# Kernel optimization log

Measured on AMD Instinct MI355X. Metric: run time of the kernel, lower is better.

The kernel has to match this reference:

```python
import jax, jax.numpy as jnp
import numpy as np

H = 16
D_MODEL = 1024
D_K = D_MODEL // H  # 64
NEG = -1e9


def setup_inputs() -> dict:
    key = jax.random.key(0)
    ks = jax.random.split(key, 9)
    nb, nw = 4, 2048
    Q = jax.random.normal(ks[0], (nb, nw, D_MODEL), dtype=jnp.float32)
    K = jax.random.normal(ks[1], (nb, nw, D_MODEL), dtype=jnp.float32)
    V = jax.random.normal(ks[2], (nb, nw, D_MODEL), dtype=jnp.float32)
    mask = jax.random.randint(ks[3], (nb, nw, nw), 0, 2, dtype=jnp.int32)
    s = 1.0 / np.sqrt(D_MODEL)
    Wq = jax.random.normal(ks[4], (D_MODEL, D_MODEL), dtype=jnp.float32) * s
    Wk = jax.random.normal(ks[5], (D_MODEL, D_MODEL), dtype=jnp.float32) * s
    Wv = jax.random.normal(ks[6], (D_MODEL, D_MODEL), dtype=jnp.float32) * s
    Wo = jax.random.normal(ks[7], (D_MODEL, D_MODEL), dtype=jnp.float32) * s
    return {"Q": Q, "K": K, "V": V, "mask": mask,
            "Wq": Wq, "Wk": Wk, "Wv": Wv, "Wo": Wo}


def reference(Q, K, V, mask, Wq, Wk, Wv, Wo):
    nb, nw, _ = Q.shape
    scaling = jnp.asarray(np.sqrt(D_K), dtype=Q.dtype)
    # nn.Linear(bias=False): y = x @ W.T; split heads -> [nb, h, nw, d_k]
    q = (Q @ Wq.T).reshape(nb, nw, H, D_K).transpose(0, 2, 1, 3)
    k = (K @ Wk.T).reshape(nb, nw, H, D_K).transpose(0, 2, 1, 3)
    v = (V @ Wv.T).reshape(nb, nw, H, D_K).transpose(0, 2, 1, 3)
    scores = jnp.einsum('bhqd,bhkd->bhqk', q, k) / scaling
    # mask broadcast over heads (unsqueeze(1) in torch)
    scores = jnp.where(mask[:, None, :, :] == 0, jnp.asarray(NEG, scores.dtype), scores)
    probs = jax.nn.softmax(scores, axis=-1)
    # dropout is identity in eval mode
    attn = jnp.einsum('bhqk,bhkd->bhqd', probs, v)
    x = attn.transpose(0, 2, 1, 3).reshape(nb, nw, D_MODEL)
    return x @ Wo.T
```

## Files before the change

### kernel.cpp

```cpp
#include <hip/hip_runtime.h>
#include <hip/hip_bf16.h>
#include <cstdint>
#include <cmath>

#define NB 4
#define NW 2048
#define DM 1024
#define NH 16
#define DK 64

typedef __attribute__((ext_vector_type(8))) short bf16x8;
typedef __attribute__((ext_vector_type(4))) float f32x4;
union cvt8 { uint4 u; __hip_bfloat16 h[8]; };

__device__ __forceinline__ void async_ld16(const void* g, void* l) {
  __builtin_amdgcn_global_load_lds((__attribute__((address_space(1))) void*)g,
                                   (__attribute__((address_space(3))) void*)l,
                                   16, 0, 0);
}

__device__ __forceinline__ unsigned short bf16bits(float x) {
  __hip_bfloat16 h = __float2bfloat16(x);
  return *(unsigned short*)&h;
}

__global__ void __launch_bounds__(256) cvt_qkv(const float* __restrict__ Q,
                                               const float* __restrict__ K,
                                               const float* __restrict__ V,
                                               __hip_bfloat16* __restrict__ Qb,
                                               __hip_bfloat16* __restrict__ Kb,
                                               __hip_bfloat16* __restrict__ Vb) {
  const float* in = blockIdx.y == 0 ? Q : (blockIdx.y == 1 ? K : V);
  __hip_bfloat16* out = blockIdx.y == 0 ? Qb : (blockIdx.y == 1 ? Kb : Vb);
  size_t i = ((size_t)blockIdx.x * 256 + threadIdx.x) * 8;
  float4 a = *(const float4*)(in + i);
  float4 b = *(const float4*)(in + i + 4);
  cvt8 c;
#pragma unroll
  for (int t = 0; t < 4; ++t) {
    c.h[t]     = __float2bfloat16(((const float*)&a)[t]);
    c.h[4 + t] = __float2bfloat16(((const float*)&b)[t]);
  }
  *(uint4*)(out + i) = c.u;
}

__global__ void __launch_bounds__(256) cvt_w(const float* __restrict__ W0,
                                             const float* __restrict__ W1,
                                             const float* __restrict__ W2,
                                             const float* __restrict__ W3,
                                             __hip_bfloat16* __restrict__ Wb) {
  const float* in = blockIdx.y == 0 ? W0 : (blockIdx.y == 1 ? W1 : (blockIdx.y == 2 ? W2 : W3));
  __hip_bfloat16* out = Wb + (size_t)blockIdx.y * DM * DM;
  size_t i = ((size_t)blockIdx.x * 256 + threadIdx.x) * 8;
  float4 a = *(const float4*)(in + i);
  float4 b = *(const float4*)(in + i + 4);
  cvt8 c;
#pragma unroll
  for (int t = 0; t < 4; ++t) {
    c.h[t]     = __float2bfloat16(((const float*)&a)[t]);
    c.h[4 + t] = __float2bfloat16(((const float*)&b)[t]);
  }
  *(uint4*)(out + i) = c.u;
}

__global__ void __launch_bounds__(256) mask_pack(const int* __restrict__ mask,
                                                 unsigned long long* __restrict__ bits) {
  int lane = threadIdx.x & 63;
  size_t tid = (size_t)blockIdx.x * blockDim.x + threadIdx.x;
  size_t widx = tid >> 6;
  int m = mask[widx * 64 + lane];
  unsigned long long b = __ballot(m != 0);
  if (lane == 0) bits[widx] = b;
}

__global__ void __launch_bounds__(256) gemm_qkv(const __hip_bfloat16* __restrict__ Qb,
                                                const __hip_bfloat16* __restrict__ Kb,
                                                const __hip_bfloat16* __restrict__ Vb,
                                                const __hip_bfloat16* __restrict__ Wb,
                                                __hip_bfloat16* __restrict__ q_ws,
                                                __hip_bfloat16* __restrict__ k_ws,
                                                __hip_bfloat16* __restrict__ vt) {
  __shared__ __align__(16) __hip_bfloat16 sA[128 * 32];
  __shared__ __align__(16) __hip_bfloat16 sB[128 * 32];
  const int z = blockIdx.z;
  const __hip_bfloat16* A = z == 0 ? Qb : (z == 1 ? Kb : Vb);
  const __hip_bfloat16* W = Wb + (size_t)z * DM * DM;
  const int tid = threadIdx.x;
  const int lane = tid & 63;
  const int l15 = lane & 15, quad = lane >> 4;
  const int rowA = blockIdx.y * 128;
  const int colB = blockIdx.x * 128;
  const int wm = ((tid >> 6) >> 1) * 64, wn = ((tid >> 6) & 1) * 64;

  const f32x4 fz = {0.f, 0.f, 0.f, 0.f};
  f32x4 acc[4][4];
#pragma unroll
  for (int i = 0; i < 4; ++i)
#pragma unroll
    for (int j = 0; j < 4; ++j) acc[i][j] = fz;

  for (int k0 = 0; k0 < DM; k0 += 32) {
#pragma unroll
    for (int j = 0; j < 2; ++j) {
      int c = j * 256 + tid;
      int r = c >> 2, col = (c & 3) * 8;
      int ldsOff = (j * 256 + (tid & ~63)) * 16;
      async_ld16(A + (size_t)(rowA + r) * DM + k0 + col, (char*)sA + ldsOff);
      async_ld16(W + (size_t)(colB + r) * DM + k0 + col, (char*)sB + ldsOff);
    }
    __syncthreads();
    bf16x8 af[4], bfr[4];
#pragma unroll
    for (int i = 0; i < 4; ++i) {
      af[i]  = *(const bf16x8*)(sA + (wm + i * 16 + l15) * 32 + quad * 8);
      bfr[i] = *(const bf16x8*)(sB + (wn + i * 16 + l15) * 32 + quad * 8);
    }
#pragma unroll
    for (int i = 0; i < 4; ++i)
#pragma unroll
      for (int j = 0; j < 4; ++j)
        acc[i][j] = __builtin_amdgcn_mfma_f32_16x16x32_bf16(af[i], bfr[j], acc[i][j], 0, 0, 0);
    __syncthreads();
  }

  if (z < 2) {
    __hip_bfloat16* C = z == 0 ? q_ws : k_ws;
    float alpha = z == 0 ? 0.125f : 1.0f;
#pragma unroll
    for (int i = 0; i < 4; ++i) {
      int row = rowA + wm + i * 16 + quad * 4;
#pragma unroll
      for (int j = 0; j < 4; ++j) {
        int col = colB + wn + j * 16 + l15;
#pragma unroll
        for (int r = 0; r < 4; ++r)
          C[(size_t)(row + r) * DM + col] = __float2bfloat16(acc[i][j][r] * alpha);
      }
    }
  } else {
#pragma unroll
    for (int i = 0; i < 4; ++i) {
      int row = rowA + wm + i * 16 + quad * 4;
      int bb = row >> 11, tok = row & 2047;
#pragma unroll
      for (int j = 0; j < 4; ++j) {
        int col = colB + wn + j * 16 + l15;
        uint2 u;
        u.x = (unsigned int)bf16bits(acc[i][j][0]) | ((unsigned int)bf16bits(acc[i][j][1]) << 16);
        u.y = (unsigned int)bf16bits(acc[i][j][2]) | ((unsigned int)bf16bits(acc[i][j][3]) << 16);
        *(uint2*)(vt + ((size_t)bb * 1024 + col) * 2048 + tok) = u;
      }
    }
  }
}

__global__ void __launch_bounds__(256) gemm_out(const __hip_bfloat16* __restrict__ A,
                                                const __hip_bfloat16* __restrict__ W,
                                                float* __restrict__ C) {
  __shared__ __align__(16) __hip_bfloat16 sA[128 * 32];
  __shared__ __align__(16) __hip_bfloat16 sB[128 * 32];
  const int tid = threadIdx.x;
  const int lane = tid & 63;
  const int l15 = lane & 15, quad = lane >> 4;
  const int rowA = blockIdx.y * 128;
  const int colB = blockIdx.x * 128;
  const int wm = ((tid >> 6) >> 1) * 64, wn = ((tid >> 6) & 1) * 64;

  const f32x4 fz = {0.f, 0.f, 0.f, 0.f};
  f32x4 acc[4][4];
#pragma unroll
  for (int i = 0; i < 4; ++i)
#pragma unroll
    for (int j = 0; j < 4; ++j) acc[i][j] = fz;

  for (int k0 = 0; k0 < DM; k0 += 32) {
#pragma unroll
    for (int j = 0; j < 2; ++j) {
      int c = j * 256 + tid;
      int r = c >> 2, col = (c & 3) * 8;
      int ldsOff = (j * 256 + (tid & ~63)) * 16;
      async_ld16(A + (size_t)(rowA + r) * DM + k0 + col, (char*)sA + ldsOff);
      async_ld16(W + (size_t)(colB + r) * DM + k0 + col, (char*)sB + ldsOff);
    }
    __syncthreads();
    bf16x8 af[4], bfr[4];
#pragma unroll
    for (int i = 0; i < 4; ++i) {
      af[i]  = *(const bf16x8*)(sA + (wm + i * 16 + l15) * 32 + quad * 8);
      bfr[i] = *(const bf16x8*)(sB + (wn + i * 16 + l15) * 32 + quad * 8);
    }
#pragma unroll
    for (int i = 0; i < 4; ++i)
#pragma unroll
      for (int j = 0; j < 4; ++j)
        acc[i][j] = __builtin_amdgcn_mfma_f32_16x16x32_bf16(af[i], bfr[j], acc[i][j], 0, 0, 0);
    __syncthreads();
  }
#pragma unroll
  for (int i = 0; i < 4; ++i) {
    int row = rowA + wm + i * 16 + quad * 4;
#pragma unroll
    for (int j = 0; j < 4; ++j) {
      int col = colB + wn + j * 16 + l15;
#pragma unroll
      for (int r = 0; r < 4; ++r)
        C[(size_t)(row + r) * DM + col] = acc[i][j][r];
    }
  }
}

#define LDSK 72

__global__ void __launch_bounds__(256) attn_fused(const __hip_bfloat16* __restrict__ q,
                                                  const __hip_bfloat16* __restrict__ kk,
                                                  const __hip_bfloat16* __restrict__ vt,
                                                  const unsigned long long* __restrict__ mbits,
                                                  __hip_bfloat16* __restrict__ o) {
  __shared__ __align__(16) __hip_bfloat16 sK[64 * LDSK];
  __shared__ __align__(16) __hip_bfloat16 sVT[64 * LDSK];
  __shared__ __align__(16) __hip_bfloat16 sP[4][16 * LDSK];

  const int tid = threadIdx.x;
  const int wave = tid >> 6, lane = tid & 63;
  const int l15 = lane & 15, quad = lane >> 4;
  const int b = blockIdx.z, h = blockIdx.y;
  const int qbase = blockIdx.x * 64 + wave * 16;

  const __hip_bfloat16* qp = q + (size_t)(b * NW + qbase + l15) * DM + h * DK + quad * 8;
  bf16x8 aq0 = *(const bf16x8*)qp;
  bf16x8 aq1 = *(const bf16x8*)(qp + 32);

  const __hip_bfloat16* vbase = vt + ((size_t)b * 1024 + h * DK) * 2048;

  const f32x4 fz = {0.f, 0.f, 0.f, 0.f};
  f32x4 oacc[4];
  float ls[4] = {0.f, 0.f, 0.f, 0.f};
#pragma unroll
  for (int i = 0; i < 4; ++i) oacc[i] = fz;

  for (int kt = 0; kt < NW / 64; ++kt) {
    __syncthreads();
#pragma unroll
    for (int j = 0; j < 2; ++j) {
      int c = j * 256 + tid;
      int r = c >> 3, col = (c & 7) * 8;
      *(uint4*)(sK + r * LDSK + col) =
          *(const uint4*)(kk + (size_t)(b * NW + kt * 64 + r) * DM + h * DK + col);
      *(uint4*)(sVT + r * LDSK + col) =
          *(const uint4*)(vbase + (size_t)r * 2048 + kt * 64 + col);
    }
    unsigned long long mw[4];
#pragma unroll
    for (int r = 0; r < 4; ++r)
      mw[r] = mbits[(size_t)(b * NW + qbase + quad * 4 + r) * (NW / 64) + kt];
    __syncthreads();

    f32x4 S[4];
#pragma unroll
    for (int nc = 0; nc < 4; ++nc) {
      bf16x8 b0 = *(const bf16x8*)(sK + (nc * 16 + l15) * LDSK + quad * 8);
      bf16x8 b1 = *(const bf16x8*)(sK + (nc * 16 + l15) * LDSK + 32 + quad * 8);
      f32x4 t = fz;
      t = __builtin_amdgcn_mfma_f32_16x16x32_bf16(aq0, b0, t, 0, 0, 0);
      t = __builtin_amdgcn_mfma_f32_16x16x32_bf16(aq1, b1, t, 0, 0, 0);
      S[nc] = t;
    }
    unsigned long long sh[4];
#pragma unroll
    for (int r = 0; r < 4; ++r) sh[r] = mw[r] >> l15;
#pragma unroll
    for (int nc = 0; nc < 4; ++nc)
#pragma unroll
      for (int r = 0; r < 4; ++r) {
        float p = __expf(S[nc][r]);
        if (!((sh[r] >> (nc * 16)) & 1ull)) p = 0.f;
        ls[r] += p;
        sP[wave][(quad * 4 + r) * LDSK + nc * 16 + l15] = __float2bfloat16(p);
      }
    __threadfence_block();

    bf16x8 ap0 = *(const bf16x8*)(&sP[wave][l15 * LDSK + quad * 8]);
    bf16x8 ap1 = *(const bf16x8*)(&sP[wave][l15 * LDSK + 32 + quad * 8]);
#pragma unroll
    for (int nc = 0; nc < 4; ++nc) {
      bf16x8 b0 = *(const bf16x8*)(sVT + (nc * 16 + l15) * LDSK + quad * 8);
      bf16x8 b1 = *(const bf16x8*)(sVT + (nc * 16 + l15) * LDSK + 32 + quad * 8);
      oacc[nc] = __builtin_amdgcn_mfma_f32_16x16x32_bf16(ap0, b0, oacc[nc], 0, 0, 0);
      oacc[nc] = __builtin_amdgcn_mfma_f32_16x16x32_bf16(ap1, b1, oacc[nc], 0, 0, 0);
    }
  }

#pragma unroll
  for (int s = 1; s < 16; s <<= 1)
#pragma unroll
    for (int r = 0; r < 4; ++r) ls[r] += __shfl_xor(ls[r], s, 64);

  float inv[4];
#pragma unroll
  for (int r = 0; r < 4; ++r) inv[r] = 1.0f / fmaxf(ls[r], 1e-30f);
#pragma unroll
  for (int nc = 0; nc < 4; ++nc)
#pragma unroll
    for (int r = 0; r < 4; ++r)
      o[(size_t)(b * NW + qbase + quad * 4 + r) * DM + h * DK + nc * 16 + l15] =
          __float2bfloat16(oacc[nc][r] * inv[r]);
}

extern "C" void kernel_launch(void* const* d_in, const int* in_sizes, int n_in,
                              void* d_out, int out_size, void* d_ws, size_t ws_size,
                              hipStream_t stream) {
  const float* Q  = (const float*)d_in[0];
  const float* K  = (const float*)d_in[1];
  const float* V  = (const float*)d_in[2];
  const int*   Mm = (const int*)d_in[3];
  const float* Wq = (const float*)d_in[4];
  const float* Wk = (const float*)d_in[5];
  const float* Wv = (const float*)d_in[6];
  const float* Wo = (const float*)d_in[7];
  float* out = (float*)d_out;

  char* ws = (char*)d_ws;
  const size_t tb = (size_t)NB * NW * DM * sizeof(__hip_bfloat16);
  const size_t wb = (size_t)DM * DM * sizeof(__hip_bfloat16);
  __hip_bfloat16* Qb   = (__hip_bfloat16*)(ws);
  __hip_bfloat16* Kb   = (__hip_bfloat16*)(ws + tb);
  __hip_bfloat16* k_ws = (__hip_bfloat16*)(ws + 2 * tb);
  __hip_bfloat16* vt   = (__hip_bfloat16*)(ws + 3 * tb);
  __hip_bfloat16* Wb   = (__hip_bfloat16*)(ws + 4 * tb);
  unsigned long long* mbits = (unsigned long long*)(ws + 4 * tb + 4 * wb);
  __hip_bfloat16* q_ws = (__hip_bfloat16*)d_out;
  __hip_bfloat16* Vb   = (__hip_bfloat16*)((char*)d_out + tb);
  __hip_bfloat16* a_ws = Qb;

  const int gq = (int)((size_t)NB * NW * DM / 8 / 256);
  const int gw = (int)((size_t)DM * DM / 8 / 256);

  mask_pack<<<(size_t)NB * NW * NW / 256, 256, 0, stream>>>(Mm, mbits);
  cvt_qkv<<<dim3(gq, 3), 256, 0, stream>>>(Q, K, V, Qb, Kb, Vb);
  cvt_w<<<dim3(gw, 4), 256, 0, stream>>>(Wq, Wk, Wv, Wo, Wb);
  gemm_qkv<<<dim3(DM / 128, NB * NW / 128, 3), 256, 0, stream>>>(Qb, Kb, Vb, Wb,
                                                                 q_ws, k_ws, vt);
  attn_fused<<<dim3(NW / 64, NH, NB), 256, 0, stream>>>(q_ws, k_ws, vt, mbits, a_ws);
  gemm_out<<<dim3(DM / 128, NB * NW / 128), 256, 0, stream>>>(a_ws, Wb + 3 * (size_t)DM * DM, out);
}
```

Measured before the change: 475.5 us.

## Process 32 query rows per wave in attention to reuse K/V tiles

Each wave in the fused attention kernel now handles two 16-row query groups, giving 128 queries per block, and the grid shrinks by half. Every K and V^T fragment loaded from LDS feeds two MFMAs, and each global K/V tile load serves twice as many queries, which halves K/V global traffic and block-level sync overhead. In exchange, register use rises from the doubled accumulators and score tiles, and there are fewer blocks (1024), which may lower occupancy and latency hiding.

```diff
diff --git a/kernel.cpp b/kernel.cpp
--- a/kernel.cpp
+++ b/kernel.cpp
@@ -218,25 +218,32 @@
                                                   __hip_bfloat16* __restrict__ o) {
   __shared__ __align__(16) __hip_bfloat16 sK[64 * LDSK];
   __shared__ __align__(16) __hip_bfloat16 sVT[64 * LDSK];
-  __shared__ __align__(16) __hip_bfloat16 sP[4][16 * LDSK];
+  __shared__ __align__(16) __hip_bfloat16 sP[4][32 * LDSK];
 
   const int tid = threadIdx.x;
   const int wave = tid >> 6, lane = tid & 63;
   const int l15 = lane & 15, quad = lane >> 4;
   const int b = blockIdx.z, h = blockIdx.y;
-  const int qbase = blockIdx.x * 64 + wave * 16;
-
-  const __hip_bfloat16* qp = q + (size_t)(b * NW + qbase + l15) * DM + h * DK + quad * 8;
-  bf16x8 aq0 = *(const bf16x8*)qp;
-  bf16x8 aq1 = *(const bf16x8*)(qp + 32);
+  const int qbase = blockIdx.x * 128 + wave * 32;
+
+  bf16x8 aq0[2], aq1[2];
+#pragma unroll
+  for (int rg = 0; rg < 2; ++rg) {
+    const __hip_bfloat16* qp =
+        q + (size_t)(b * NW + qbase + rg * 16 + l15) * DM + h * DK + quad * 8;
+    aq0[rg] = *(const bf16x8*)qp;
+    aq1[rg] = *(const bf16x8*)(qp + 32);
+  }
 
   const __hip_bfloat16* vbase = vt + ((size_t)b * 1024 + h * DK) * 2048;
 
   const f32x4 fz = {0.f, 0.f, 0.f, 0.f};
-  f32x4 oacc[4];
-  float ls[4] = {0.f, 0.f, 0.f, 0.f};
-#pragma unroll
-  for (int i = 0; i < 4; ++i) oacc[i] = fz;
+  f32x4 oacc[2][4];
+  float ls[2][4];
+#pragma unroll
+  for (int rg = 0; rg < 2; ++rg)
+#pragma unroll
+    for (int i = 0; i < 4; ++i) { oacc[rg][i] = fz; ls[rg][i] = 0.f; }
 
   for (int kt = 0; kt < NW / 64; ++kt) {
     __syncthreads();
@@ -249,61 +256,81 @@
       *(uint4*)(sVT + r * LDSK + col) =
           *(const uint4*)(vbase + (size_t)r * 2048 + kt * 64 + col);
     }
-    unsigned long long mw[4];
-#pragma unroll
-    for (int r = 0; r < 4; ++r)
-      mw[r] = mbits[(size_t)(b * NW + qbase + quad * 4 + r) * (NW / 64) + kt];
-    __syncthreads();
-
-    f32x4 S[4];
+    unsigned long long mw[2][4];
+#pragma unroll
+    for (int rg = 0; rg < 2; ++rg)
+#pragma unroll
+      for (int r = 0; r < 4; ++r)
+        mw[rg][r] = mbits[(size_t)(b * NW + qbase + rg * 16 + quad * 4 + r) * (NW / 64) + kt];
+    __syncthreads();
+
+    f32x4 S[2][4];
 #pragma unroll
     for (int nc = 0; nc < 4; ++nc) {
-      bf16x8 b0 = *(const bf16x8*)(sK + (nc * 16 + l15) * LDSK + quad * 8);
-      bf16x8 b1 = *(const bf16x8*)(sK + (nc * 16 + l15) * LDSK + 32 + quad * 8);
-      f32x4 t = fz;
-      t = __builtin_amdgcn_mfma_f32_16x16x32_bf16(aq0, b0, t, 0, 0, 0);
-      t = __builtin_amdgcn_mfma_f32_16x16x32_bf16(aq1, b1, t, 0, 0, 0);
-      S[nc] = t;
-    }
-    unsigned long long sh[4];
-#pragma unroll
-    for (int r = 0; r < 4; ++r) sh[r] = mw[r] >> l15;
+      bf16x8 kb0 = *(const bf16x8*)(sK + (nc * 16 + l15) * LDSK + quad * 8);
+      bf16x8 kb1 = *(const bf16x8*)(sK + (nc * 16 + l15) * LDSK + 32 + quad * 8);
+#pragma unroll
+      for (int rg = 0; rg < 2; ++rg) {
+        f32x4 t = fz;
+        t = __builtin_amdgcn_mfma_f32_16x16x32_bf16(aq0[rg], kb0, t, 0, 0, 0);
+        t = __builtin_amdgcn_mfma_f32_16x16x32_bf16(aq1[rg], kb1, t, 0, 0, 0);
+        S[rg][nc] = t;
+      }
+    }
+#pragma unroll
+    for (int rg = 0; rg < 2; ++rg) {
+      unsigned long long sh[4];
+#pragma unroll
+      for (int r = 0; r < 4; ++r) sh[r] = mw[rg][r] >> l15;
+#pragma unroll
+      for (int nc = 0; nc < 4; ++nc)
+#pragma unroll
+        for (int r = 0; r < 4; ++r) {
+          float p = __expf(S[rg][nc][r]);
+          if (!((sh[r] >> (nc * 16)) & 1ull)) p = 0.f;
+          ls[rg][r] += p;
+          sP[wave][(rg * 16 + quad * 4 + r) * LDSK + nc * 16 + l15] = __float2bfloat16(p);
+        }
+    }
+    __threadfence_block();
+
+    bf16x8 ap0[2], ap1[2];
+#pragma unroll
+    for (int rg = 0; rg < 2; ++rg) {
+      ap0[rg] = *(const bf16x8*)(&sP[wave][(rg * 16 + l15) * LDSK + quad * 8]);
+      ap1[rg] = *(const bf16x8*)(&sP[wave][(rg * 16 + l15) * LDSK + 32 + quad * 8]);
+    }
+#pragma unroll
+    for (int nc = 0; nc < 4; ++nc) {
+      bf16x8 vb0 = *(const bf16x8*)(sVT + (nc * 16 + l15) * LDSK + quad * 8);
+      bf16x8 vb1 = *(const bf16x8*)(sVT + (nc * 16 + l15) * LDSK + 32 + quad * 8);
+#pragma unroll
+      for (int rg = 0; rg < 2; ++rg) {
+        oacc[rg][nc] = __builtin_amdgcn_mfma_f32_16x16x32_bf16(ap0[rg], vb0, oacc[rg][nc], 0, 0, 0);
+        oacc[rg][nc] = __builtin_amdgcn_mfma_f32_16x16x32_bf16(ap1[rg], vb1, oacc[rg][nc], 0, 0, 0);
+      }
+    }
+  }
+
+#pragma unroll
+  for (int s = 1; s < 16; s <<= 1)
+#pragma unroll
+    for (int rg = 0; rg < 2; ++rg)
+#pragma unroll
+      for (int r = 0; r < 4; ++r) ls[rg][r] += __shfl_xor(ls[rg][r], s, 64);
+
+#pragma unroll
+  for (int rg = 0; rg < 2; ++rg) {
+    float inv[4];
+#pragma unroll
+    for (int r = 0; r < 4; ++r) inv[r] = 1.0f / fmaxf(ls[rg][r], 1e-30f);
 #pragma unroll
     for (int nc = 0; nc < 4; ++nc)
 #pragma unroll
-      for (int r = 0; r < 4; ++r) {
-        float p = __expf(S[nc][r]);
-        if (!((sh[r] >> (nc * 16)) & 1ull)) p = 0.f;
-        ls[r] += p;
-        sP[wave][(quad * 4 + r) * LDSK + nc * 16 + l15] = __float2bfloat16(p);
-      }
-    __threadfence_block();
-
-    bf16x8 ap0 = *(const bf16x8*)(&sP[wave][l15 * LDSK + quad * 8]);
-    bf16x8 ap1 = *(const bf16x8*)(&sP[wave][l15 * LDSK + 32 + quad * 8]);
-#pragma unroll
-    for (int nc = 0; nc < 4; ++nc) {
-      bf16x8 b0 = *(const bf16x8*)(sVT + (nc * 16 + l15) * LDSK + quad * 8);
-      bf16x8 b1 = *(const bf16x8*)(sVT + (nc * 16 + l15) * LDSK + 32 + quad * 8);
-      oacc[nc] = __builtin_amdgcn_mfma_f32_16x16x32_bf16(ap0, b0, oacc[nc], 0, 0, 0);
-      oacc[nc] = __builtin_amdgcn_mfma_f32_16x16x32_bf16(ap1, b1, oacc[nc], 0, 0, 0);
-    }
-  }
-
-#pragma unroll
-  for (int s = 1; s < 16; s <<= 1)
-#pragma unroll
-    for (int r = 0; r < 4; ++r) ls[r] += __shfl_xor(ls[r], s, 64);
-
-  float inv[4];
-#pragma unroll
-  for (int r = 0; r < 4; ++r) inv[r] = 1.0f / fmaxf(ls[r], 1e-30f);
-#pragma unroll
-  for (int nc = 0; nc < 4; ++nc)
-#pragma unroll
-    for (int r = 0; r < 4; ++r)
-      o[(size_t)(b * NW + qbase + quad * 4 + r) * DM + h * DK + nc * 16 + l15] =
-          __float2bfloat16(oacc[nc][r] * inv[r]);
+      for (int r = 0; r < 4; ++r)
+        o[(size_t)(b * NW + qbase + rg * 16 + quad * 4 + r) * DM + h * DK + nc * 16 + l15] =
+            __float2bfloat16(oacc[rg][nc][r] * inv[r]);
+  }
 }
 
 extern "C" void kernel_launch(void* const* d_in, const int* in_sizes, int n_in,
@@ -340,6 +367,6 @@
   cvt_w<<<dim3(gw, 4), 256, 0, stream>>>(Wq, Wk, Wv, Wo, Wb);
   gemm_qkv<<<dim3(DM / 128, NB * NW / 128, 3), 256, 0, stream>>>(Qb, Kb, Vb, Wb,
                                                                  q_ws, k_ws, vt);
-  attn_fused<<<dim3(NW / 64, NH, NB), 256, 0, stream>>>(q_ws, k_ws, vt, mbits, a_ws);
+  attn_fused<<<dim3(NW / 128, NH, NB), 256, 0, stream>>>(q_ws, k_ws, vt, mbits, a_ws);
   gemm_out<<<dim3(DM / 128, NB * NW / 128), 256, 0, stream>>>(a_ws, Wb + 3 * (size_t)DM * DM, out);
 }
```

Result: slower. 516.6 us (+8.6%).
